# Performance work log

Measured on AMD Instinct MI355X. Metric: run time of the kernel, lower is better.

The kernel has to match this reference:

```python
import jax, jax.numpy as jnp
import numpy as np

NUM_EMBEDDINGS = 4096
EMBEDDING_DIM = 256
COMMITMENT_COST = 0.25


def setup_inputs() -> dict:
    key = jax.random.key(0)
    k1, k2 = jax.random.split(key)
    x = jax.random.normal(k1, (64, 32, 32, EMBEDDING_DIM), dtype=jnp.float32)
    # torch init: uniform(-1/K, 1/K)
    codebook = jax.random.uniform(
        k2, (NUM_EMBEDDINGS, EMBEDDING_DIM), dtype=jnp.float32,
        minval=-1.0 / NUM_EMBEDDINGS, maxval=1.0 / NUM_EMBEDDINGS)
    return {"x": x, "codebook": codebook}


def reference(x, codebook):
    D = codebook.shape[1]
    flat_x = x.reshape(-1, D)                                   # [N, D]
    distances = (jnp.sum(flat_x ** 2, axis=1, keepdims=True)
                 + jnp.sum(codebook ** 2, axis=1)
                 - 2.0 * flat_x @ codebook.T)                   # [N, K]
    encoding_indices = jnp.argmin(distances, axis=1)            # [N]
    quantized = codebook[encoding_indices].reshape(x.shape)     # gather (== one-hot matmul)
    q_sg = jax.lax.stop_gradient(quantized)
    x_sg = jax.lax.stop_gradient(x)
    commitment_loss = jnp.mean((q_sg - x) ** 2)
    codebook_loss = jnp.mean((quantized - x_sg) ** 2)
    vq_loss = codebook_loss + COMMITMENT_COST * commitment_loss
    # straight-through estimator
    quantized_st = x + jax.lax.stop_gradient(quantized - x)
    return quantized_st, vq_loss
```

## Files before the change

kernel.cpp:

```cpp
#include <hip/hip_runtime.h>
#include <stdint.h>

#define DIM     256
#define NCODES  4096
#define NROWS   65536
#define ROWS_WG 128
#define CCOLS   64
#define NCH     (NCODES / CCOLS)
#define CHB     (CCOLS * DIM)

#define OFF_BIMG  0u
#define OFF_HC    (1u << 20)
#define OFF_IDX   ((1u << 20) + 16384u)
#define OFF_PART  (OFF_IDX + 262144u)

typedef __attribute__((ext_vector_type(8)))  int   i32x8;
typedef __attribute__((ext_vector_type(16))) float f32x16;
typedef const __attribute__((address_space(1))) uint32_t* gas1_t;
typedef __attribute__((address_space(3))) uint32_t*       las3_t;

__device__ __forceinline__ uint32_t pk4(float a, float b, float c, float d) {
  uint32_t lo = (uint32_t)__builtin_amdgcn_cvt_pk_fp8_f32(a, b, 0, false) & 0xFFFFu;
  uint32_t hi = (uint32_t)__builtin_amdgcn_cvt_pk_fp8_f32(c, d, 0, false) & 0xFFFFu;
  return lo | (hi << 16);
}

__global__ __launch_bounds__(64) void k1_prep(const float* __restrict__ cb,
                                              uint8_t* __restrict__ ws) {
  const int code = blockIdx.x;
  const int l = threadIdx.x;
  float4 v = ((const float4*)(cb + (size_t)code * DIM))[l];
  float ax = v.x * 4096.0f, ay = v.y * 4096.0f;
  float az = v.z * 4096.0f, aw = v.w * 4096.0f;
  uint32_t off = (uint32_t)(code >> 6) * (uint32_t)CHB
               + (uint32_t)(l >> 2) * 1024u
               + (uint32_t)(code & 63) * 16u + (uint32_t)(l & 3) * 4u;
  *(uint32_t*)(ws + OFF_BIMG + off) = pk4(ax, ay, az, aw);
  float s = ax * ax + ay * ay + az * az + aw * aw;
  #pragma unroll
  for (int m = 1; m < 64; m <<= 1) s += __shfl_xor(s, m, 64);
  if (l == 0) ((float*)(ws + OFF_HC))[code] = 512.0f + s * (1.0f / 8192.0f);
}

__global__ __launch_bounds__(256, 2) void k2_argmin(const float* __restrict__ x,
                                                    uint8_t* __restrict__ ws) {
  __shared__ uint4 smem4[2048];
  char* smem = (char*)&smem4[0];
  const int t = threadIdx.x;
  const int wave = t >> 6;
  const int lane = t & 63;
  const int c = lane & 31;
  const int g = lane >> 5;
  const int wg = blockIdx.x;
  const uint8_t* __restrict__ Bimg = ws + OFF_BIMG;
  const float* __restrict__ hcg = (const float*)(ws + OFF_HC);
  int* bidx = (int*)(ws + OFF_IDX);

  const int rbw = (wave >> 1) * 64;
  const int cbw = (wave & 1) * 32;

  {
    const float* xb = x + (size_t)wg * ROWS_WG * DIM;
    #pragma unroll
    for (int it = 0; it < 16; ++it) {
      int u = it * 256 + t;
      int row = u >> 5;
      int k8 = u & 31;
      const float4* src = (const float4*)(xb + (size_t)row * DIM + k8 * 8);
      float4 v0 = src[0], v1 = src[1];
      uint32_t* d = (uint32_t*)(smem + (k8 >> 2) * 4096 + row * 32 + (k8 & 3) * 8);
      d[0] = pk4(-v0.x, -v0.y, -v0.z, -v0.w);
      d[1] = pk4(-v1.x, -v1.y, -v1.z, -v1.w);
    }
  }
  __syncthreads();

  i32x8 a[2][4];
  #pragma unroll
  for (int rt = 0; rt < 2; ++rt)
    #pragma unroll
    for (int ks = 0; ks < 4; ++ks)
      a[rt][ks] = *(const i32x8*)(smem + (ks * 2 + g) * 4096
                                  + (rbw + rt * 32 + c) * 32);
  __syncthreads();

  auto stageB = [&](int buf, int ch) {
    const uint8_t* gsrc = Bimg + (size_t)ch * CHB + (size_t)t * 16;
    char* lb = smem + buf * 16384 + (t & 192) * 16;
    #pragma unroll
    for (int i = 0; i < 4; ++i)
      __builtin_amdgcn_global_load_lds((gas1_t)(uintptr_t)(gsrc + i * 4096),
                                       (las3_t)(uintptr_t)(lb + i * 4096),
                                       16, 0, 0);
  };

  uint32_t key[2][16];
  #pragma unroll
  for (int rt = 0; rt < 2; ++rt)
    #pragma unroll
    for (int r = 0; r < 16; ++r) key[rt][r] = 0xFFFFFFFFu;

  const int hoff = cbw + c;
  const uint32_t maskhi = 0xFFFFF000u;

  const int ch0 = ((wg * 7) + ((wg >> 8) * 29)) & 63;

  stageB(0, ch0);
  float h_cur = hcg[ch0 * CCOLS + hoff];

  for (int i = 0; i < NCH; ++i) {
    const int cur = i & 1;
    const int ch = (ch0 + i) & 63;
    const int chn = (ch0 + i + 1) & 63;
    __syncthreads();
    if (i + 1 < NCH) stageB(cur ^ 1, chn);
    float h_nxt = hcg[chn * CCOLS + hoff];

    f32x16 acc0, acc1;
    #pragma unroll
    for (int j = 0; j < 16; ++j) { acc0[j] = h_cur; acc1[j] = h_cur; }
    const char* bb = smem + cur * 16384 + (cbw + c) * 16;
    #pragma unroll
    for (int ks = 0; ks < 4; ++ks) {
      uint4 b0 = *(const uint4*)(bb + (ks * 4 + g * 2) * 1024);
      uint4 b1 = *(const uint4*)(bb + (ks * 4 + g * 2 + 1) * 1024);
      i32x8 b;
      b[0] = (int)b0.x; b[1] = (int)b0.y; b[2] = (int)b0.z; b[3] = (int)b0.w;
      b[4] = (int)b1.x; b[5] = (int)b1.y; b[6] = (int)b1.z; b[7] = (int)b1.w;
      acc0 = __builtin_amdgcn_mfma_scale_f32_32x32x64_f8f6f4(
                 a[0][ks], b, acc0, 0, 0, 0, 0x7F7F7F7F, 0, 0x7F7F7F7F);
      acc1 = __builtin_amdgcn_mfma_scale_f32_32x32x64_f8f6f4(
                 a[1][ks], b, acc1, 0, 0, 0, 0x7F7F7F7F, 0, 0x7F7F7F7F);
    }
    const uint32_t col = (uint32_t)(ch * CCOLS + hoff);
    #pragma unroll
    for (int r = 0; r < 16; ++r) {
      key[0][r] = min(key[0][r], (__float_as_uint(acc0[r]) & maskhi) | col);
      key[1][r] = min(key[1][r], (__float_as_uint(acc1[r]) & maskhi) | col);
    }
    h_cur = h_nxt;
  }

  #pragma unroll
  for (int rt = 0; rt < 2; ++rt)
    #pragma unroll
    for (int r = 0; r < 16; ++r) {
      uint32_t k = key[rt][r];
      #pragma unroll
      for (int m = 1; m < 32; m <<= 1) {
        uint32_t ko = (uint32_t)__shfl_xor((int)k, m, 32);
        k = min(k, ko);
      }
      key[rt][r] = k;
    }

  uint32_t* bk = (uint32_t*)smem;
  __syncthreads();
  if (t < 128) bk[t] = 0xFFFFFFFFu;
  __syncthreads();
  if (c == 0) {
    #pragma unroll
    for (int rt = 0; rt < 2; ++rt)
      #pragma unroll
      for (int r = 0; r < 16; ++r) {
        int rl = rbw + rt * 32 + (r & 3) + ((r >> 2) << 3) + (g << 2);
        atomicMin(&bk[rl], key[rt][r]);
      }
  }
  __syncthreads();
  if (t < 128) bidx[wg * ROWS_WG + t] = (int)(bk[t] & 0xFFFu);
}

__global__ __launch_bounds__(256) void k3_finalize(const float* __restrict__ x,
                                                   const float* __restrict__ cb,
                                                   uint8_t* __restrict__ ws,
                                                   float* __restrict__ out) {
  const int t = threadIdx.x;
  const size_t i4 = (size_t)blockIdx.x * 256 + t;
  const int row = (int)(i4 >> 6);
  const int k4 = (int)(i4 & 63);
  const int* bidx = (const int*)(ws + OFF_IDX);
  const int code = bidx[row] & (NCODES - 1);
  float4 q = ((const float4*)(cb + (size_t)code * DIM))[k4];
  float4 xv = ((const float4*)x)[i4];
  ((float4*)out)[i4] = q;
  float dx = q.x - xv.x, dy = q.y - xv.y, dz = q.z - xv.z, dw = q.w - xv.w;
  float p = dx * dx + dy * dy + dz * dz + dw * dw;
  #pragma unroll
  for (int m = 1; m < 64; m <<= 1) p += __shfl_xor(p, m, 64);
  __shared__ float ps[4];
  if ((t & 63) == 0) ps[t >> 6] = p;
  __syncthreads();
  if (t == 0)
    ((float*)(ws + OFF_PART))[blockIdx.x] = ps[0] + ps[1] + ps[2] + ps[3];
}

__global__ __launch_bounds__(256) void k4_loss(const uint8_t* __restrict__ ws,
                                               float* __restrict__ out,
                                               int out_size) {
  const float* part = (const float*)(ws + OFF_PART);
  float s = 0.0f;
  for (int i = threadIdx.x; i < 16384; i += 256) s += part[i];
  #pragma unroll
  for (int m = 1; m < 64; m <<= 1) s += __shfl_xor(s, m, 64);
  __shared__ float ps[4];
  if ((threadIdx.x & 63) == 0) ps[threadIdx.x >> 6] = s;
  __syncthreads();
  if (threadIdx.x == 0)
    out[out_size - 1] =
        1.25f * (ps[0] + ps[1] + ps[2] + ps[3]) * (1.0f / 16777216.0f);
}

extern "C" void kernel_launch(void* const* d_in, const int* in_sizes, int n_in,
                              void* d_out, int out_size, void* d_ws, size_t ws_size,
                              hipStream_t stream) {
  const float* x = (const float*)d_in[0];
  const float* cb = (const float*)d_in[1];
  uint8_t* ws = (uint8_t*)d_ws;
  float* out = (float*)d_out;

  k1_prep<<<dim3(NCODES), dim3(64), 0, stream>>>(cb, ws);
  k2_argmin<<<dim3(NROWS / ROWS_WG), dim3(256), 0, stream>>>(x, ws);
  k3_finalize<<<dim3(16384), dim3(256), 0, stream>>>(x, cb, ws, out);
  k4_loss<<<dim3(1), dim3(256), 0, stream>>>(ws, out, out_size);
}
```

Baseline: 203.2 us.

## Split codebook search across two workgroups per row block and fuse loss reduction

The argmin kernel now launches twice as many workgroups, each scanning half of the codebook for the same 128-row tile, and writes packed distance/index keys per half. The finalize kernel takes the min of the two keys per row. The separate loss kernel is folded into finalize through a last-block atomic counter, and launch bounds are raised to allow more waves per CU. This is meant to fix a 512-workgroup grid that underfills the GPU and to remove one launch, at the cost of loading and converting each x tile twice and a serialized final reduction in one block.

```diff
diff --git a/kernel.cpp b/kernel.cpp
--- a/kernel.cpp
+++ b/kernel.cpp
@@ -6,13 +6,14 @@
 #define NROWS   65536
 #define ROWS_WG 128
 #define CCOLS   64
-#define NCH     (NCODES / CCOLS)
+#define NCHB    32
 #define CHB     (CCOLS * DIM)
 
 #define OFF_BIMG  0u
 #define OFF_HC    (1u << 20)
-#define OFF_IDX   ((1u << 20) + 16384u)
-#define OFF_PART  (OFF_IDX + 262144u)
+#define OFF_KEYS  ((1u << 20) + 16384u)
+#define OFF_PART  (OFF_KEYS + 524288u)
+#define OFF_CNT   (OFF_PART + 65536u)
 
 typedef __attribute__((ext_vector_type(8)))  int   i32x8;
 typedef __attribute__((ext_vector_type(16))) float f32x16;
@@ -29,6 +30,7 @@
                                               uint8_t* __restrict__ ws) {
   const int code = blockIdx.x;
   const int l = threadIdx.x;
+  if (code == 0 && l == 0) *(uint32_t*)(ws + OFF_CNT) = 0u;
   float4 v = ((const float4*)(cb + (size_t)code * DIM))[l];
   float ax = v.x * 4096.0f, ay = v.y * 4096.0f;
   float az = v.z * 4096.0f, aw = v.w * 4096.0f;
@@ -42,7 +44,7 @@
   if (l == 0) ((float*)(ws + OFF_HC))[code] = 512.0f + s * (1.0f / 8192.0f);
 }
 
-__global__ __launch_bounds__(256, 2) void k2_argmin(const float* __restrict__ x,
+__global__ __launch_bounds__(256, 4) void k2_argmin(const float* __restrict__ x,
                                                     uint8_t* __restrict__ ws) {
   __shared__ uint4 smem4[2048];
   char* smem = (char*)&smem4[0];
@@ -52,15 +54,16 @@
   const int c = lane & 31;
   const int g = lane >> 5;
   const int wg = blockIdx.x;
+  const int rg = wg >> 1;
+  const int half = wg & 1;
   const uint8_t* __restrict__ Bimg = ws + OFF_BIMG;
   const float* __restrict__ hcg = (const float*)(ws + OFF_HC);
-  int* bidx = (int*)(ws + OFF_IDX);
 
   const int rbw = (wave >> 1) * 64;
   const int cbw = (wave & 1) * 32;
 
   {
-    const float* xb = x + (size_t)wg * ROWS_WG * DIM;
+    const float* xb = x + (size_t)rg * ROWS_WG * DIM;
     #pragma unroll
     for (int it = 0; it < 16; ++it) {
       int u = it * 256 + t;
@@ -103,17 +106,18 @@
   const int hoff = cbw + c;
   const uint32_t maskhi = 0xFFFFF000u;
 
-  const int ch0 = ((wg * 7) + ((wg >> 8) * 29)) & 63;
-
-  stageB(0, ch0);
-  float h_cur = hcg[ch0 * CCOLS + hoff];
-
-  for (int i = 0; i < NCH; ++i) {
+  const int ch0 = ((wg * 7) + ((wg >> 8) * 11)) & 31;
+  const int chbase = half * NCHB;
+
+  stageB(0, chbase + ch0);
+  float h_cur = hcg[(chbase + ch0) * CCOLS + hoff];
+
+  for (int i = 0; i < NCHB; ++i) {
     const int cur = i & 1;
-    const int ch = (ch0 + i) & 63;
-    const int chn = (ch0 + i + 1) & 63;
+    const int ch = chbase + ((ch0 + i) & 31);
+    const int chn = chbase + ((ch0 + i + 1) & 31);
     __syncthreads();
-    if (i + 1 < NCH) stageB(cur ^ 1, chn);
+    if (i + 1 < NCHB) stageB(cur ^ 1, chn);
     float h_nxt = hcg[chn * CCOLS + hoff];
 
     f32x16 acc0, acc1;
@@ -168,19 +172,21 @@
       }
   }
   __syncthreads();
-  if (t < 128) bidx[wg * ROWS_WG + t] = (int)(bk[t] & 0xFFFu);
+  uint32_t* keyout = (uint32_t*)(ws + OFF_KEYS) + (size_t)half * 65536 + rg * ROWS_WG;
+  if (t < 128) keyout[t] = bk[t];
 }
 
 __global__ __launch_bounds__(256) void k3_finalize(const float* __restrict__ x,
                                                    const float* __restrict__ cb,
                                                    uint8_t* __restrict__ ws,
-                                                   float* __restrict__ out) {
+                                                   float* __restrict__ out,
+                                                   int out_size) {
   const int t = threadIdx.x;
   const size_t i4 = (size_t)blockIdx.x * 256 + t;
   const int row = (int)(i4 >> 6);
   const int k4 = (int)(i4 & 63);
-  const int* bidx = (const int*)(ws + OFF_IDX);
-  const int code = bidx[row] & (NCODES - 1);
+  const uint32_t* keys = (const uint32_t*)(ws + OFF_KEYS);
+  const int code = (int)(min(keys[row], keys[65536 + row]) & 0xFFFu);
   float4 q = ((const float4*)(cb + (size_t)code * DIM))[k4];
   float4 xv = ((const float4*)x)[i4];
   ((float4*)out)[i4] = q;
@@ -189,26 +195,28 @@
   #pragma unroll
   for (int m = 1; m < 64; m <<= 1) p += __shfl_xor(p, m, 64);
   __shared__ float ps[4];
+  __shared__ bool amLast;
   if ((t & 63) == 0) ps[t >> 6] = p;
   __syncthreads();
-  if (t == 0)
+  if (t == 0) {
     ((float*)(ws + OFF_PART))[blockIdx.x] = ps[0] + ps[1] + ps[2] + ps[3];
-}
-
-__global__ __launch_bounds__(256) void k4_loss(const uint8_t* __restrict__ ws,
-                                               float* __restrict__ out,
-                                               int out_size) {
-  const float* part = (const float*)(ws + OFF_PART);
-  float s = 0.0f;
-  for (int i = threadIdx.x; i < 16384; i += 256) s += part[i];
-  #pragma unroll
-  for (int m = 1; m < 64; m <<= 1) s += __shfl_xor(s, m, 64);
-  __shared__ float ps[4];
-  if ((threadIdx.x & 63) == 0) ps[threadIdx.x >> 6] = s;
-  __syncthreads();
-  if (threadIdx.x == 0)
-    out[out_size - 1] =
-        1.25f * (ps[0] + ps[1] + ps[2] + ps[3]) * (1.0f / 16777216.0f);
+    __threadfence();
+    amLast = (atomicAdd((uint32_t*)(ws + OFF_CNT), 1u) == 16383u);
+  }
+  __syncthreads();
+  if (amLast) {
+    __threadfence();
+    const float* part = (const float*)(ws + OFF_PART);
+    float s = 0.0f;
+    for (int i = t; i < 16384; i += 256) s += part[i];
+    #pragma unroll
+    for (int m = 1; m < 64; m <<= 1) s += __shfl_xor(s, m, 64);
+    if ((t & 63) == 0) ps[t >> 6] = s;
+    __syncthreads();
+    if (t == 0)
+      out[out_size - 1] =
+          1.25f * (ps[0] + ps[1] + ps[2] + ps[3]) * (1.0f / 16777216.0f);
+  }
 }
 
 extern "C" void kernel_launch(void* const* d_in, const int* in_sizes, int n_in,
@@ -220,7 +228,6 @@
   float* out = (float*)d_out;
 
   k1_prep<<<dim3(NCODES), dim3(64), 0, stream>>>(cb, ws);
-  k2_argmin<<<dim3(NROWS / ROWS_WG), dim3(256), 0, stream>>>(x, ws);
-  k3_finalize<<<dim3(16384), dim3(256), 0, stream>>>(x, cb, ws, out);
-  k4_loss<<<dim3(1), dim3(256), 0, stream>>>(ws, out, out_size);
-}
+  k2_argmin<<<dim3(NROWS / ROWS_WG * 2), dim3(256), 0, stream>>>(x, ws);
+  k3_finalize<<<dim3(16384), dim3(256), 0, stream>>>(x, cb, ws, out, out_size);
+}
```

New measurement: 767.9 us. 278% more time.

## Fuse gather and loss partial into argmin kernel, drop finalize kernel

Applied to the files above, without the earlier changes.

The codebook gather, output write and squared-error partial sum move into the tail of the argmin kernel, using the per-row indices already held in shared memory. This removes the separate finalize launch, the global index buffer round trip and the 16384-entry partial array, so the loss kernel now sums only 512 partials. In exchange, each argmin workgroup does a serial memory-bound tail after its compute, and with only 512 workgroups at 2 per CU that tail may not overlap well with other workgroups' MFMA work. The x rows re-read here were read earlier by the same workgroup, so they may still be in cache.

```diff
diff --git a/kernel.cpp b/kernel.cpp
--- a/kernel.cpp
+++ b/kernel.cpp
@@ -11,8 +11,7 @@
 
 #define OFF_BIMG  0u
 #define OFF_HC    (1u << 20)
-#define OFF_IDX   ((1u << 20) + 16384u)
-#define OFF_PART  (OFF_IDX + 262144u)
+#define OFF_PART  ((1u << 20) + 16384u)
 
 typedef __attribute__((ext_vector_type(8)))  int   i32x8;
 typedef __attribute__((ext_vector_type(16))) float f32x16;
@@ -43,7 +42,9 @@
 }
 
 __global__ __launch_bounds__(256, 2) void k2_argmin(const float* __restrict__ x,
-                                                    uint8_t* __restrict__ ws) {
+                                                    const float* __restrict__ cb,
+                                                    uint8_t* __restrict__ ws,
+                                                    float* __restrict__ out) {
   __shared__ uint4 smem4[2048];
   char* smem = (char*)&smem4[0];
   const int t = threadIdx.x;
@@ -54,13 +55,12 @@
   const int wg = blockIdx.x;
   const uint8_t* __restrict__ Bimg = ws + OFF_BIMG;
   const float* __restrict__ hcg = (const float*)(ws + OFF_HC);
-  int* bidx = (int*)(ws + OFF_IDX);
 
   const int rbw = (wave >> 1) * 64;
   const int cbw = (wave & 1) * 32;
 
+  const float* xb = x + (size_t)wg * ROWS_WG * DIM;
   {
-    const float* xb = x + (size_t)wg * ROWS_WG * DIM;
     #pragma unroll
     for (int it = 0; it < 16; ++it) {
       int u = it * 256 + t;
@@ -168,31 +168,29 @@
       }
   }
   __syncthreads();
-  if (t < 128) bidx[wg * ROWS_WG + t] = (int)(bk[t] & 0xFFFu);
-}
-
-__global__ __launch_bounds__(256) void k3_finalize(const float* __restrict__ x,
-                                                   const float* __restrict__ cb,
-                                                   uint8_t* __restrict__ ws,
-                                                   float* __restrict__ out) {
-  const int t = threadIdx.x;
-  const size_t i4 = (size_t)blockIdx.x * 256 + t;
-  const int row = (int)(i4 >> 6);
-  const int k4 = (int)(i4 & 63);
-  const int* bidx = (const int*)(ws + OFF_IDX);
-  const int code = bidx[row] & (NCODES - 1);
-  float4 q = ((const float4*)(cb + (size_t)code * DIM))[k4];
-  float4 xv = ((const float4*)x)[i4];
-  ((float4*)out)[i4] = q;
-  float dx = q.x - xv.x, dy = q.y - xv.y, dz = q.z - xv.z, dw = q.w - xv.w;
-  float p = dx * dx + dy * dy + dz * dz + dw * dw;
-  #pragma unroll
-  for (int m = 1; m < 64; m <<= 1) p += __shfl_xor(p, m, 64);
+
+  float* ob = out + (size_t)wg * ROWS_WG * DIM;
+  float psum = 0.0f;
+  #pragma unroll 4
+  for (int it = 0; it < 32; ++it) {
+    int u = it * 256 + t;
+    int row = u >> 6;
+    int k4i = u & 63;
+    int code = (int)(bk[row] & 0xFFFu);
+    float4 q = ((const float4*)(cb + (size_t)code * DIM))[k4i];
+    float4 xv = ((const float4*)xb)[u];
+    ((float4*)ob)[u] = q;
+    float dx = q.x - xv.x, dy = q.y - xv.y;
+    float dz = q.z - xv.z, dw = q.w - xv.w;
+    psum += dx * dx + dy * dy + dz * dz + dw * dw;
+  }
+  #pragma unroll
+  for (int m = 1; m < 64; m <<= 1) psum += __shfl_xor(psum, m, 64);
   __shared__ float ps[4];
-  if ((t & 63) == 0) ps[t >> 6] = p;
+  if (lane == 0) ps[wave] = psum;
   __syncthreads();
   if (t == 0)
-    ((float*)(ws + OFF_PART))[blockIdx.x] = ps[0] + ps[1] + ps[2] + ps[3];
+    ((float*)(ws + OFF_PART))[wg] = ps[0] + ps[1] + ps[2] + ps[3];
 }
 
 __global__ __launch_bounds__(256) void k4_loss(const uint8_t* __restrict__ ws,
@@ -200,7 +198,7 @@
                                                int out_size) {
   const float* part = (const float*)(ws + OFF_PART);
   float s = 0.0f;
-  for (int i = threadIdx.x; i < 16384; i += 256) s += part[i];
+  for (int i = threadIdx.x; i < 512; i += 256) s += part[i];
   #pragma unroll
   for (int m = 1; m < 64; m <<= 1) s += __shfl_xor(s, m, 64);
   __shared__ float ps[4];
@@ -220,7 +218,6 @@
   float* out = (float*)d_out;
 
   k1_prep<<<dim3(NCODES), dim3(64), 0, stream>>>(cb, ws);
-  k2_argmin<<<dim3(NROWS / ROWS_WG), dim3(256), 0, stream>>>(x, ws);
-  k3_finalize<<<dim3(16384), dim3(256), 0, stream>>>(x, cb, ws, out);
+  k2_argmin<<<dim3(NROWS / ROWS_WG), dim3(256), 0, stream>>>(x, cb, ws, out);
   k4_loss<<<dim3(1), dim3(256), 0, stream>>>(ws, out, out_size);
 }
```

Result: faster. 180.5 us (-11.1%).
